# Kernel optimization log

Measured on AMD Instinct MI355X. Metric: run time of the kernel, lower is better.

Reference implementation:

```python
import jax, jax.numpy as jnp
import numpy as np

EMBED = 512
HEADS = 8
HEAD_LEN = EMBED // HEADS  # 64


def setup_inputs() -> dict:
    key = jax.random.key(0)
    ks = jax.random.split(key, 8)
    B, L = 8, 2048
    return {
        "query": jax.random.normal(ks[0], (B, L, EMBED), dtype=jnp.float32),
        "key": jax.random.normal(ks[1], (B, L, EMBED), dtype=jnp.float32),
        "value": jax.random.normal(ks[2], (B, L, EMBED), dtype=jnp.float32),
        "Wq": jax.random.normal(ks[3], (HEAD_LEN, HEAD_LEN), dtype=jnp.float32) * 0.05,
        "Wk": jax.random.normal(ks[4], (HEAD_LEN, HEAD_LEN), dtype=jnp.float32) * 0.05,
        "Wv": jax.random.normal(ks[5], (HEAD_LEN, HEAD_LEN), dtype=jnp.float32) * 0.05,
        "Wo": jax.random.normal(ks[6], (EMBED, EMBED), dtype=jnp.float32) * 0.05,
        "bo": jax.random.normal(ks[7], (EMBED,), dtype=jnp.float32) * 0.05,
    }


def reference(query, key, value, Wq, Wk, Wv, Wo, bo):
    B, Lq, E = query.shape
    Lk = key.shape[1]
    Lv = value.shape[1]
    H, d = HEADS, HEAD_LEN
    # Faithful to original: q/k reshaped to (B, H, L, d) (splits the sequence
    # dim, not the feature dim); v reshaped to (B, L, H, d).
    q = query.reshape(B, H, Lq, d) @ Wq.T   # nn.Linear: x @ W^T
    k = key.reshape(B, H, Lk, d) @ Wk.T
    v = value.reshape(B, Lv, H, d) @ Wv.T
    scores = jnp.einsum('bhqf,bhkf->bhqk', q, k) / (E ** 0.5)  # scale = sqrt(embed_size)
    w = jax.nn.softmax(scores, axis=3)
    out = jnp.einsum('bhql,blhd->bqhd', w, v).reshape(B, Lq, H * d)
    return out @ Wo.T + bo
```

## Files before the change

kernel.cpp:

```cpp
#include <hip/hip_runtime.h>
#include <stdint.h>

#define BB 8
#define LL 2048
#define EE 512
#define HH 8
#define DD 64

typedef __attribute__((ext_vector_type(8))) short short8;
typedef __attribute__((ext_vector_type(4))) float f32x4;
typedef __attribute__((ext_vector_type(16))) float f32x16;
typedef __attribute__((ext_vector_type(2))) unsigned int u32x2v;

#define QSCALE 0.06376435773361453f

__device__ __forceinline__ uint32_t pk2bf(float a, float b) {
    union { float f; uint32_t u; } va, vb; va.f = a; vb.f = b;
    return __builtin_amdgcn_perm(vb.u + 0x8000u, va.u + 0x8000u, 0x07060302u);
}

__device__ __forceinline__ short8 pack8(const float4 t0, const float4 t1) {
    union { uint32_t u[4]; short8 s; } r;
    r.u[0] = pk2bf(t0.x, t0.y); r.u[1] = pk2bf(t0.z, t0.w);
    r.u[2] = pk2bf(t1.x, t1.y); r.u[3] = pk2bf(t1.z, t1.w);
    return r.s;
}

__global__ __launch_bounds__(256) void prep_weights(const float* __restrict__ Wq, const float* __restrict__ Wk,
                                                    const float* __restrict__ Wv, const float* __restrict__ Wo,
                                                    short* __restrict__ WqB, short* __restrict__ WkB,
                                                    short* __restrict__ WvB, short* __restrict__ WoB) {
    int i = blockIdx.x * 256 + threadIdx.x;
    const float* src; short* dst; int off;
    if (i < 1024)      { src = Wq; dst = WqB; off = i; }
    else if (i < 2048) { src = Wk; dst = WkB; off = i - 1024; }
    else if (i < 3072) { src = Wv; dst = WvB; off = i - 2048; }
    else               { src = Wo; dst = WoB; off = i - 3072; }
    float4 t = reinterpret_cast<const float4*>(src)[off];
    uint2 d; d.x = pk2bf(t.x, t.y); d.y = pk2bf(t.z, t.w);
    reinterpret_cast<uint2*>(dst)[off] = d;
}

__global__ __launch_bounds__(256) void proj_fused(const float* __restrict__ query, const float* __restrict__ key,
                                                  const float* __restrict__ value,
                                                  const short* __restrict__ WqB, const short* __restrict__ WkB,
                                                  const short* __restrict__ WvB,
                                                  short* __restrict__ Oq, short* __restrict__ Ok, short* __restrict__ OvT) {
    const int id = blockIdx.x;
    const int lane = threadIdx.x & 63;
    const int wave = threadIdx.x >> 6;
    const int quad = lane >> 4;
    const int c    = lane & 15;

    if (id < 4096) {
        const bool isq = id < 2048;
        const float* X = isq ? query : key;
        const short* W = isq ? WqB : WkB;
        short* O = isq ? Oq : Ok;
        const float oscale = isq ? QSCALE : 1.0f;
        const int xid = isq ? id : id - 2048;
        const long r0 = (long)xid * 64 + wave * 16;

        short8 xb[2];
#pragma unroll
        for (int kk = 0; kk < 2; ++kk) {
            const float* src = X + (r0 + c) * 64 + kk * 32 + quad * 8;
            xb[kk] = pack8(*reinterpret_cast<const float4*>(src), *reinterpret_cast<const float4*>(src + 4));
        }

        f32x4 acc[4];
#pragma unroll
        for (int ft = 0; ft < 4; ++ft) { acc[ft][0]=0.f; acc[ft][1]=0.f; acc[ft][2]=0.f; acc[ft][3]=0.f; }

#pragma unroll
        for (int ft = 0; ft < 4; ++ft)
#pragma unroll
            for (int kk = 0; kk < 2; ++kk) {
                short8 wa = *reinterpret_cast<const short8*>(W + (ft * 16 + c) * 64 + kk * 32 + quad * 8);
                acc[ft] = __builtin_amdgcn_mfma_f32_16x16x32_bf16(wa, xb[kk], acc[ft], 0, 0, 0);
            }

#pragma unroll
        for (int ft = 0; ft < 4; ++ft) {
            uint2 d;
            d.x = pk2bf(acc[ft][0] * oscale, acc[ft][1] * oscale);
            d.y = pk2bf(acc[ft][2] * oscale, acc[ft][3] * oscale);
            *reinterpret_cast<uint2*>(O + (r0 + c) * 64 + ft * 16 + quad * 4) = d;
        }
    } else {
        const int vid = id - 4096;
        const int bh = vid >> 5, lt = vid & 31;
        const int b = bh >> 3, h = bh & 7;
        const int l0 = lt * 64 + wave * 16;

        short8 xa[2];
#pragma unroll
        for (int kk = 0; kk < 2; ++kk) {
            const float* src = value + ((long)(b * LL + l0 + c) * EE + h * 64) + kk * 32 + quad * 8;
            xa[kk] = pack8(*reinterpret_cast<const float4*>(src), *reinterpret_cast<const float4*>(src + 4));
        }

        f32x4 acc[4];
#pragma unroll
        for (int nt = 0; nt < 4; ++nt) { acc[nt][0]=0.f; acc[nt][1]=0.f; acc[nt][2]=0.f; acc[nt][3]=0.f; }

#pragma unroll
        for (int nt = 0; nt < 4; ++nt)
#pragma unroll
            for (int kk = 0; kk < 2; ++kk) {
                short8 wb = *reinterpret_cast<const short8*>(WvB + (nt * 16 + c) * 64 + kk * 32 + quad * 8);
                acc[nt] = __builtin_amdgcn_mfma_f32_16x16x32_bf16(xa[kk], wb, acc[nt], 0, 0, 0);
            }

#pragma unroll
        for (int nt = 0; nt < 4; ++nt) {
            uint2 d;
            d.x = pk2bf(acc[nt][0], acc[nt][1]);
            d.y = pk2bf(acc[nt][2], acc[nt][3]);
            *reinterpret_cast<uint2*>(OvT + ((long)bh * 64 + nt * 16 + c) * LL + l0 + quad * 4) = d;
        }
    }
}

__global__ __launch_bounds__(256, 2) void attn_kernel(const short* __restrict__ Q, const short* __restrict__ K,
                                                      const short* __restrict__ VT, short* __restrict__ Oattn) {
    const int lane = threadIdx.x & 63;
    const int wave = threadIdx.x >> 6;
    const int hl = lane >> 5;
    const int c  = lane & 31;
    const int bh = blockIdx.x & 63;
    const int qs = blockIdx.x >> 6;
    const int b = bh >> 3, head = bh & 7;
    const int q0 = qs * 256 + wave * 64;

    short8 aq[2][4];
#pragma unroll
    for (int t = 0; t < 2; ++t)
#pragma unroll
        for (int ks = 0; ks < 4; ++ks)
            aq[t][ks] = *reinterpret_cast<const short8*>(Q + ((long)bh * LL + q0 + t * 32 + c) * 64 + ks * 16 + hl * 8);

    f32x16 of[2][2];
#pragma unroll
    for (int t = 0; t < 2; ++t)
#pragma unroll
        for (int ft = 0; ft < 2; ++ft)
#pragma unroll
            for (int i = 0; i < 16; ++i) of[t][ft][i] = 0.f;
    float l[2] = {0.f, 0.f};

    const short* Kb = K  + (long)bh * LL * 64;
    const short* Vb = VT + (long)bh * 64 * LL;

    for (int kb = 0; kb < LL; kb += 64) {
        short8 kf[2][4], vf[2][4];
#pragma unroll
        for (int kt = 0; kt < 2; ++kt)
#pragma unroll
            for (int ks = 0; ks < 4; ++ks)
                kf[kt][ks] = *reinterpret_cast<const short8*>(Kb + (long)(kb + kt * 32 + c) * 64 + ks * 16 + hl * 8);
#pragma unroll
        for (int ft = 0; ft < 2; ++ft)
#pragma unroll
            for (int kk = 0; kk < 4; ++kk)
                vf[ft][kk] = *reinterpret_cast<const short8*>(Vb + (long)(ft * 32 + c) * LL + kb + kk * 16 + hl * 8);

#pragma unroll
        for (int t = 0; t < 2; ++t)
#pragma unroll
            for (int kt = 0; kt < 2; ++kt) {
                f32x16 s;
#pragma unroll
                for (int i = 0; i < 16; ++i) s[i] = 0.f;
#pragma unroll
                for (int ks = 0; ks < 4; ++ks)
                    s = __builtin_amdgcn_mfma_f32_32x32x16_bf16(kf[kt][ks], aq[t][ks], s, 0, 0, 0);

                uint32_t xd[4][2];
                float lac = 0.f;
#pragma unroll
                for (int g = 0; g < 4; ++g) {
                    const float p0 = __builtin_amdgcn_exp2f(s[4 * g + 0]);
                    const float p1 = __builtin_amdgcn_exp2f(s[4 * g + 1]);
                    const float p2 = __builtin_amdgcn_exp2f(s[4 * g + 2]);
                    const float p3 = __builtin_amdgcn_exp2f(s[4 * g + 3]);
                    lac += (p0 + p1) + (p2 + p3);
                    xd[g][0] = pk2bf(p0, p1);
                    xd[g][1] = pk2bf(p2, p3);
                }
                l[t] += lac;

#pragma unroll
                for (int kt2 = 0; kt2 < 2; ++kt2) {
                    u32x2v rA = __builtin_amdgcn_permlane32_swap(xd[2 * kt2][0], xd[2 * kt2 + 1][0], false, false);
                    u32x2v rB = __builtin_amdgcn_permlane32_swap(xd[2 * kt2][1], xd[2 * kt2 + 1][1], false, false);
                    union { uint32_t u[4]; short8 s8; } pb;
                    pb.u[0] = rA[0]; pb.u[1] = rB[0]; pb.u[2] = rA[1]; pb.u[3] = rB[1];
                    const int kk = kt * 2 + kt2;
                    of[t][0] = __builtin_amdgcn_mfma_f32_32x32x16_bf16(vf[0][kk], pb.s8, of[t][0], 0, 0, 0);
                    of[t][1] = __builtin_amdgcn_mfma_f32_32x32x16_bf16(vf[1][kk], pb.s8, of[t][1], 0, 0, 0);
                }
            }
    }

    float inv[2];
#pragma unroll
    for (int t = 0; t < 2; ++t) {
        l[t] += __shfl_xor(l[t], 32);
        inv[t] = 1.0f / l[t];
    }

#pragma unroll
    for (int t = 0; t < 2; ++t) {
        const long row = (long)b * LL + q0 + t * 32 + c;
#pragma unroll
        for (int ft = 0; ft < 2; ++ft)
#pragma unroll
            for (int g = 0; g < 4; ++g) {
                const float v0 = of[t][ft][4 * g + 0] * inv[t], v1 = of[t][ft][4 * g + 1] * inv[t];
                const float v2 = of[t][ft][4 * g + 2] * inv[t], v3 = of[t][ft][4 * g + 3] * inv[t];
                uint2 d; d.x = pk2bf(v0, v1); d.y = pk2bf(v2, v3);
                *reinterpret_cast<uint2*>(Oattn + row * EE + head * 64 + ft * 32 + g * 8 + hl * 4) = d;
            }
    }
}

__global__ __launch_bounds__(256) void out_proj(const short* __restrict__ A, const short* __restrict__ WoB,
                                                const float* __restrict__ bo, float* __restrict__ out) {
    const int lane = threadIdx.x & 63;
    const int wave = threadIdx.x >> 6;
    const int quad = lane >> 4;
    const int c    = lane & 15;
    const int nb = blockIdx.x;
    const int rb = blockIdx.y;
    const long r0 = (long)rb * 64 + wave * 16;

    f32x4 acc[4];
#pragma unroll
    for (int ft = 0; ft < 4; ++ft) { acc[ft][0]=0.f; acc[ft][1]=0.f; acc[ft][2]=0.f; acc[ft][3]=0.f; }

    for (int ks = 0; ks < 16; ++ks) {
        short8 bfr = *reinterpret_cast<const short8*>(A + (r0 + c) * EE + ks * 32 + quad * 8);
#pragma unroll
        for (int ft = 0; ft < 4; ++ft) {
            short8 afr = *reinterpret_cast<const short8*>(WoB + ((long)(nb * 64 + ft * 16 + c)) * EE + ks * 32 + quad * 8);
            acc[ft] = __builtin_amdgcn_mfma_f32_16x16x32_bf16(afr, bfr, acc[ft], 0, 0, 0);
        }
    }

#pragma unroll
    for (int ft = 0; ft < 4; ++ft) {
        float4 bias = *reinterpret_cast<const float4*>(bo + nb * 64 + ft * 16 + quad * 4);
        float4 res;
        res.x = acc[ft][0] + bias.x; res.y = acc[ft][1] + bias.y;
        res.z = acc[ft][2] + bias.z; res.w = acc[ft][3] + bias.w;
        *reinterpret_cast<float4*>(out + (r0 + c) * EE + nb * 64 + ft * 16 + quad * 4) = res;
    }
}

extern "C" void kernel_launch(void* const* d_in, const int* in_sizes, int n_in,
                              void* d_out, int out_size, void* d_ws, size_t ws_size,
                              hipStream_t stream) {
    const float* query = (const float*)d_in[0];
    const float* key   = (const float*)d_in[1];
    const float* value = (const float*)d_in[2];
    const float* Wq    = (const float*)d_in[3];
    const float* Wk    = (const float*)d_in[4];
    const float* Wv    = (const float*)d_in[5];
    const float* Wo    = (const float*)d_in[6];
    const float* bo    = (const float*)d_in[7];
    float* out = (float*)d_out;

    char* ws = (char*)d_ws;
    const size_t SZ = 16777216;
    short* q_ws    = (short*)(ws);
    short* k_ws    = (short*)(ws + SZ);
    short* vT_ws   = (short*)(ws + 2 * SZ);
    short* attn_ws = (short*)(ws + 3 * SZ);
    short* wo_ws   = (short*)(ws + 4 * SZ);
    short* wq_ws   = (short*)(ws + 4 * SZ + 524288);
    short* wk_ws   = (short*)(ws + 4 * SZ + 532480);
    short* wv_ws   = (short*)(ws + 4 * SZ + 540672);

    prep_weights<<<268, 256, 0, stream>>>(Wq, Wk, Wv, Wo, wq_ws, wk_ws, wv_ws, wo_ws);
    proj_fused<<<6144, 256, 0, stream>>>(query, key, value, wq_ws, wk_ws, wv_ws, q_ws, k_ws, vT_ws);
    attn_kernel<<<512, 256, 0, stream>>>(q_ws, k_ws, vT_ws, attn_ws);
    out_proj<<<dim3(8, 256), 256, 0, stream>>>(attn_ws, wo_ws, bo, out);
}
```

Before: 360.0 us.

## Split attention over key halves and add a combine kernel

The attention kernel now splits the key sequence into two halves, launching twice as many blocks and allowing four blocks per CU. Each block writes unnormalized bf16 partial outputs and row sums, and a new combine kernel adds the two partials and normalizes. This is meant to raise occupancy and parallelism in the dominant attention stage. In exchange it adds extra global memory traffic, an extra launch, and bf16 rounding of the partial sums.

```diff
diff --git a/kernel.cpp b/kernel.cpp
--- a/kernel.cpp
+++ b/kernel.cpp
@@ -24,6 +24,13 @@
     r.u[0] = pk2bf(t0.x, t0.y); r.u[1] = pk2bf(t0.z, t0.w);
     r.u[2] = pk2bf(t1.x, t1.y); r.u[3] = pk2bf(t1.z, t1.w);
     return r.s;
+}
+
+__device__ __forceinline__ float bf_lo(uint32_t u) {
+    union { uint32_t u; float f; } v; v.u = u << 16; return v.f;
+}
+__device__ __forceinline__ float bf_hi(uint32_t u) {
+    union { uint32_t u; float f; } v; v.u = u & 0xffff0000u; return v.f;
 }
 
 __global__ __launch_bounds__(256) void prep_weights(const float* __restrict__ Wq, const float* __restrict__ Wk,
@@ -122,14 +129,16 @@
     }
 }
 
-__global__ __launch_bounds__(256, 2) void attn_kernel(const short* __restrict__ Q, const short* __restrict__ K,
-                                                      const short* __restrict__ VT, short* __restrict__ Oattn) {
+__global__ __launch_bounds__(256, 4) void attn_kernel(const short* __restrict__ Q, const short* __restrict__ K,
+                                                      const short* __restrict__ VT, short* __restrict__ Opart,
+                                                      float* __restrict__ lws) {
     const int lane = threadIdx.x & 63;
     const int wave = threadIdx.x >> 6;
     const int hl = lane >> 5;
     const int c  = lane & 31;
     const int bh = blockIdx.x & 63;
-    const int qs = blockIdx.x >> 6;
+    const int qs = (blockIdx.x >> 6) & 7;
+    const int split = blockIdx.x >> 9;
     const int b = bh >> 3, head = bh & 7;
     const int q0 = qs * 256 + wave * 64;
 
@@ -152,7 +161,8 @@
     const short* Kb = K  + (long)bh * LL * 64;
     const short* Vb = VT + (long)bh * 64 * LL;
 
-    for (int kb = 0; kb < LL; kb += 64) {
+    const int kb0 = split * 1024;
+    for (int kb = kb0; kb < kb0 + 1024; kb += 64) {
         short8 kf[2][4], vf[2][4];
 #pragma unroll
         for (int kt = 0; kt < 2; ++kt)
@@ -203,13 +213,15 @@
             }
     }
 
-    float inv[2];
-#pragma unroll
-    for (int t = 0; t < 2; ++t) {
-        l[t] += __shfl_xor(l[t], 32);
-        inv[t] = 1.0f / l[t];
-    }
-
+#pragma unroll
+    for (int t = 0; t < 2; ++t) l[t] += __shfl_xor(l[t], 32);
+    if (hl == 0) {
+        float* lp = lws + (long)split * (64 * LL) + bh * LL + q0;
+        lp[c] = l[0];
+        lp[32 + c] = l[1];
+    }
+
+    short* Od = Opart + (long)split * (BB * LL * EE);
 #pragma unroll
     for (int t = 0; t < 2; ++t) {
         const long row = (long)b * LL + q0 + t * 32 + c;
@@ -217,12 +229,35 @@
         for (int ft = 0; ft < 2; ++ft)
 #pragma unroll
             for (int g = 0; g < 4; ++g) {
-                const float v0 = of[t][ft][4 * g + 0] * inv[t], v1 = of[t][ft][4 * g + 1] * inv[t];
-                const float v2 = of[t][ft][4 * g + 2] * inv[t], v3 = of[t][ft][4 * g + 3] * inv[t];
-                uint2 d; d.x = pk2bf(v0, v1); d.y = pk2bf(v2, v3);
-                *reinterpret_cast<uint2*>(Oattn + row * EE + head * 64 + ft * 32 + g * 8 + hl * 4) = d;
+                uint2 d;
+                d.x = pk2bf(of[t][ft][4 * g + 0], of[t][ft][4 * g + 1]);
+                d.y = pk2bf(of[t][ft][4 * g + 2], of[t][ft][4 * g + 3]);
+                *reinterpret_cast<uint2*>(Od + row * EE + head * 64 + ft * 32 + g * 8 + hl * 4) = d;
             }
     }
+}
+
+__global__ __launch_bounds__(256) void combine_attn(const short* __restrict__ Opart, const float* __restrict__ lws,
+                                                    short* __restrict__ Oattn) {
+    const int g = blockIdx.x * 256 + threadIdx.x;
+    const int row = g >> 6;
+    const int f0  = (g & 63) * 8;
+    const int bh  = ((row >> 11) << 3) + (f0 >> 6);
+    const int rl  = row & (LL - 1);
+    const float l0 = lws[(long)bh * LL + rl];
+    const float l1 = lws[(long)64 * LL + (long)bh * LL + rl];
+    const float inv = 1.0f / (l0 + l1);
+
+    union { short8 s; uint32_t u[4]; } x0, x1, o;
+    x0.s = reinterpret_cast<const short8*>(Opart)[g];
+    x1.s = reinterpret_cast<const short8*>(Opart + (long)BB * LL * EE)[g];
+#pragma unroll
+    for (int d = 0; d < 4; ++d) {
+        const float lo = bf_lo(x0.u[d]) + bf_lo(x1.u[d]);
+        const float hi = bf_hi(x0.u[d]) + bf_hi(x1.u[d]);
+        o.u[d] = pk2bf(lo * inv, hi * inv);
+    }
+    reinterpret_cast<short8*>(Oattn)[g] = o.s;
 }
 
 __global__ __launch_bounds__(256) void out_proj(const short* __restrict__ A, const short* __restrict__ WoB,
@@ -276,14 +311,17 @@
     short* q_ws    = (short*)(ws);
     short* k_ws    = (short*)(ws + SZ);
     short* vT_ws   = (short*)(ws + 2 * SZ);
-    short* attn_ws = (short*)(ws + 3 * SZ);
-    short* wo_ws   = (short*)(ws + 4 * SZ);
-    short* wq_ws   = (short*)(ws + 4 * SZ + 524288);
-    short* wk_ws   = (short*)(ws + 4 * SZ + 532480);
-    short* wv_ws   = (short*)(ws + 4 * SZ + 540672);
+    short* op_ws   = (short*)(ws + 3 * SZ);
+    float* l_ws    = (float*)(ws + 5 * SZ);
+    short* attn_ws = q_ws;
+    short* wo_ws   = (short*)(ws + 5 * SZ + 2097152);
+    short* wq_ws   = (short*)(ws + 5 * SZ + 2097152 + 524288);
+    short* wk_ws   = (short*)(ws + 5 * SZ + 2097152 + 532480);
+    short* wv_ws   = (short*)(ws + 5 * SZ + 2097152 + 540672);
 
     prep_weights<<<268, 256, 0, stream>>>(Wq, Wk, Wv, Wo, wq_ws, wk_ws, wv_ws, wo_ws);
     proj_fused<<<6144, 256, 0, stream>>>(query, key, value, wq_ws, wk_ws, wv_ws, q_ws, k_ws, vT_ws);
-    attn_kernel<<<512, 256, 0, stream>>>(q_ws, k_ws, vT_ws, attn_ws);
+    attn_kernel<<<1024, 256, 0, stream>>>(q_ws, k_ws, vT_ws, op_ws, l_ws);
+    combine_attn<<<4096, 256, 0, stream>>>(op_ws, l_ws, attn_ws);
     out_proj<<<dim3(8, 256), 256, 0, stream>>>(attn_ws, wo_ws, bo, out);
 }
```

Measured after the change: 712.7 us. 1.98x slower.

## Software-pipeline K tile loads with double-buffered registers in attention loop

Applied to the files above, without the earlier changes.

Restructures the attention key loop into a two-stage register double buffer. The next K tile is prefetched while the current tile's MFMAs and exp run, and sched_barriers pin the load and compute order. This is meant to hide global-load latency behind compute. It costs more VGPRs, which may pressure occupancy at launch bounds of 2 waves per SIMD, and it does one redundant wrapped K load on the last iteration.

```diff
diff --git a/kernel.cpp b/kernel.cpp
--- a/kernel.cpp
+++ b/kernel.cpp
@@ -122,6 +122,44 @@
     }
 }
 
+#define LOADKF(dst, kbrow) { \
+    _Pragma("unroll") for (int kt_ = 0; kt_ < 2; ++kt_) \
+    _Pragma("unroll") for (int ks_ = 0; ks_ < 4; ++ks_) \
+        dst[kt_][ks_] = *reinterpret_cast<const short8*>(Kb + (long)((kbrow) + kt_ * 32 + c) * 64 + ks_ * 16 + hl * 8); }
+
+#define LOADVF(dst, kbcol) { \
+    _Pragma("unroll") for (int ft_ = 0; ft_ < 2; ++ft_) \
+    _Pragma("unroll") for (int kk_ = 0; kk_ < 4; ++kk_) \
+        dst[ft_][kk_] = *reinterpret_cast<const short8*>(Vb + (long)(ft_ * 32 + c) * LL + (kbcol) + kk_ * 16 + hl * 8); }
+
+#define TILE(kf, vfr) { \
+    _Pragma("unroll") for (int t = 0; t < 2; ++t) \
+    _Pragma("unroll") for (int kt = 0; kt < 2; ++kt) { \
+        f32x16 s; \
+        _Pragma("unroll") for (int i = 0; i < 16; ++i) s[i] = 0.f; \
+        _Pragma("unroll") for (int ks = 0; ks < 4; ++ks) \
+            s = __builtin_amdgcn_mfma_f32_32x32x16_bf16(kf[kt][ks], aq[t][ks], s, 0, 0, 0); \
+        uint32_t xd[4][2]; float lac = 0.f; \
+        _Pragma("unroll") for (int g = 0; g < 4; ++g) { \
+            const float p0 = __builtin_amdgcn_exp2f(s[4 * g + 0]); \
+            const float p1 = __builtin_amdgcn_exp2f(s[4 * g + 1]); \
+            const float p2 = __builtin_amdgcn_exp2f(s[4 * g + 2]); \
+            const float p3 = __builtin_amdgcn_exp2f(s[4 * g + 3]); \
+            lac += (p0 + p1) + (p2 + p3); \
+            xd[g][0] = pk2bf(p0, p1); xd[g][1] = pk2bf(p2, p3); \
+        } \
+        l[t] += lac; \
+        _Pragma("unroll") for (int kt2 = 0; kt2 < 2; ++kt2) { \
+            u32x2v rA = __builtin_amdgcn_permlane32_swap(xd[2 * kt2][0], xd[2 * kt2 + 1][0], false, false); \
+            u32x2v rB = __builtin_amdgcn_permlane32_swap(xd[2 * kt2][1], xd[2 * kt2 + 1][1], false, false); \
+            union { uint32_t u[4]; short8 s8; } pb; \
+            pb.u[0] = rA[0]; pb.u[1] = rB[0]; pb.u[2] = rA[1]; pb.u[3] = rB[1]; \
+            const int kk = kt * 2 + kt2; \
+            of[t][0] = __builtin_amdgcn_mfma_f32_32x32x16_bf16(vfr[0][kk], pb.s8, of[t][0], 0, 0, 0); \
+            of[t][1] = __builtin_amdgcn_mfma_f32_32x32x16_bf16(vfr[1][kk], pb.s8, of[t][1], 0, 0, 0); \
+        } \
+    } }
+
 __global__ __launch_bounds__(256, 2) void attn_kernel(const short* __restrict__ Q, const short* __restrict__ K,
                                                       const short* __restrict__ VT, short* __restrict__ Oattn) {
     const int lane = threadIdx.x & 63;
@@ -152,55 +190,19 @@
     const short* Kb = K  + (long)bh * LL * 64;
     const short* Vb = VT + (long)bh * 64 * LL;
 
-    for (int kb = 0; kb < LL; kb += 64) {
-        short8 kf[2][4], vf[2][4];
-#pragma unroll
-        for (int kt = 0; kt < 2; ++kt)
-#pragma unroll
-            for (int ks = 0; ks < 4; ++ks)
-                kf[kt][ks] = *reinterpret_cast<const short8*>(Kb + (long)(kb + kt * 32 + c) * 64 + ks * 16 + hl * 8);
-#pragma unroll
-        for (int ft = 0; ft < 2; ++ft)
-#pragma unroll
-            for (int kk = 0; kk < 4; ++kk)
-                vf[ft][kk] = *reinterpret_cast<const short8*>(Vb + (long)(ft * 32 + c) * LL + kb + kk * 16 + hl * 8);
-
-#pragma unroll
-        for (int t = 0; t < 2; ++t)
-#pragma unroll
-            for (int kt = 0; kt < 2; ++kt) {
-                f32x16 s;
-#pragma unroll
-                for (int i = 0; i < 16; ++i) s[i] = 0.f;
-#pragma unroll
-                for (int ks = 0; ks < 4; ++ks)
-                    s = __builtin_amdgcn_mfma_f32_32x32x16_bf16(kf[kt][ks], aq[t][ks], s, 0, 0, 0);
-
-                uint32_t xd[4][2];
-                float lac = 0.f;
-#pragma unroll
-                for (int g = 0; g < 4; ++g) {
-                    const float p0 = __builtin_amdgcn_exp2f(s[4 * g + 0]);
-                    const float p1 = __builtin_amdgcn_exp2f(s[4 * g + 1]);
-                    const float p2 = __builtin_amdgcn_exp2f(s[4 * g + 2]);
-                    const float p3 = __builtin_amdgcn_exp2f(s[4 * g + 3]);
-                    lac += (p0 + p1) + (p2 + p3);
-                    xd[g][0] = pk2bf(p0, p1);
-                    xd[g][1] = pk2bf(p2, p3);
-                }
-                l[t] += lac;
-
-#pragma unroll
-                for (int kt2 = 0; kt2 < 2; ++kt2) {
-                    u32x2v rA = __builtin_amdgcn_permlane32_swap(xd[2 * kt2][0], xd[2 * kt2 + 1][0], false, false);
-                    u32x2v rB = __builtin_amdgcn_permlane32_swap(xd[2 * kt2][1], xd[2 * kt2 + 1][1], false, false);
-                    union { uint32_t u[4]; short8 s8; } pb;
-                    pb.u[0] = rA[0]; pb.u[1] = rB[0]; pb.u[2] = rA[1]; pb.u[3] = rB[1];
-                    const int kk = kt * 2 + kt2;
-                    of[t][0] = __builtin_amdgcn_mfma_f32_32x32x16_bf16(vf[0][kk], pb.s8, of[t][0], 0, 0, 0);
-                    of[t][1] = __builtin_amdgcn_mfma_f32_32x32x16_bf16(vf[1][kk], pb.s8, of[t][1], 0, 0, 0);
-                }
-            }
+    short8 kfA[2][4], kfB[2][4], vf[2][4];
+    LOADKF(kfA, 0);
+
+#pragma unroll 1
+    for (int kb = 0; kb < LL; kb += 128) {
+        LOADVF(vf, kb);
+        LOADKF(kfB, kb + 64);
+        __builtin_amdgcn_sched_barrier(0);
+        TILE(kfA, vf);
+        LOADVF(vf, kb + 64);
+        LOADKF(kfA, (kb + 128) & (LL - 1));
+        __builtin_amdgcn_sched_barrier(0);
+        TILE(kfB, vf);
     }
 
     float inv[2];
```

New measurement: 436.4 us. 1.21x slower.
